# Kernel optimization log

Measured on AMD Instinct MI355X. Metric: run time of the kernel, lower is better.

## Reference

```python
import jax, jax.numpy as jnp
import numpy as np

VOCAB, D_MODEL, N_EXPERTS, TOP_K = 32000, 768, 8, 2
D_FF = 4 * D_MODEL
BATCH, SEQ = 2, 2048


def setup_inputs() -> dict:
    key = jax.random.key(0)
    ks = jax.random.split(key, 6)
    s = 0.02
    return {
        "x": jax.random.randint(ks[0], (BATCH, SEQ), 0, VOCAB),
        "emb": jax.random.normal(ks[1], (VOCAB, D_MODEL), jnp.float32) * s,
        "gate_w": jax.random.normal(ks[2], (D_MODEL, N_EXPERTS), jnp.float32) * s,
        "gate_b": jnp.zeros((N_EXPERTS,), jnp.float32),
        "exp_w": jax.random.normal(ks[3], (N_EXPERTS, D_MODEL, D_FF), jnp.float32) * s,
        "exp_b": jnp.zeros((N_EXPERTS, D_FF), jnp.float32),
        "head_w": jax.random.normal(ks[4], (D_FF, VOCAB), jnp.float32) * s,
        "head_b": jnp.zeros((VOCAB,), jnp.float32),
    }


def reference(x, emb, gate_w, gate_b, exp_w, exp_b, head_w, head_b):
    B, S = x.shape
    h = emb[x]                                   # [B,S,D] embedding gather
    t = h.reshape(B * S, -1)                     # [T,D] token view
    logits = t @ gate_w + gate_b                 # [T,E] router
    topv, topi = jax.lax.top_k(logits, TOP_K)    # top-2 routing
    w = jax.nn.softmax(topv, axis=-1)            # renormalized gate weights
    T = t.shape[0]
    gates = jnp.zeros_like(logits).at[jnp.arange(T)[:, None], topi].set(w)  # [T,E]
    # expert FFN: Linear(d_model -> 4*d_model) + ReLU, dense over experts
    exp_out = jax.nn.relu(jnp.einsum('td,edf->tef', t, exp_w) + exp_b)      # [T,E,F]
    moe = jnp.einsum('te,tef->tf', gates, exp_out)                          # combine
    out = moe @ head_w + head_b                  # [T,V]
    return out.reshape(B, S, -1)
```

## Files before the change

kernel.cpp:

```cpp
#include <hip/hip_runtime.h>

typedef unsigned short u16;
typedef __attribute__((ext_vector_type(8))) short short8;
typedef __attribute__((ext_vector_type(4))) float f32x4;

#define T_TOKENS 4096
#define DMODEL   768
#define DFF      3072
#define NEXP     8
#define NVOCAB   32000

#define EMB_BLOCKS   T_TOKENS
#define TEXP_BX      (DFF / 64)
#define TEXP_BY      (DMODEL / 64)
#define TEXP_BLOCKS  (TEXP_BX * TEXP_BY * NEXP)
#define THEAD_BX     (NVOCAB / 64)
#define THEAD_BY     (DFF / 64)
#define THEAD_BLOCKS (THEAD_BX * THEAD_BY)
#define FRONT_BLOCKS (EMB_BLOCKS + TEXP_BLOCKS + THEAD_BLOCKS)

__device__ __forceinline__ u16 f2bf(float f) {
  unsigned u = __float_as_uint(f);
  u += 0x7FFFu + ((u >> 16) & 1u);
  return (u16)(u >> 16);
}
__device__ __forceinline__ float bf2f(u16 b) {
  return __uint_as_float(((unsigned)b) << 16);
}

__device__ __forceinline__ void async_load16(const void* g, void* lds) {
  __builtin_amdgcn_global_load_lds((const __attribute__((address_space(1))) void*)g,
                                   (__attribute__((address_space(3))) void*)lds, 16, 0, 0);
}

#define SBAR() __builtin_amdgcn_s_barrier()
#define VMCNT(n) asm volatile("s_waitcnt vmcnt(" #n ")")
#define SCHEDB() __builtin_amdgcn_sched_barrier(0)

__device__ __forceinline__ short8 frag(const u16* buf, int row, int kc) {
  return *(const short8*)(buf + (row * 8 + (kc ^ (row & 7))) * 8);
}

__global__ __launch_bounds__(256) void k_front(
    const int* __restrict__ x, const float* __restrict__ emb,
    const float* __restrict__ gw, const float* __restrict__ gb,
    u16* __restrict__ tbf, int* __restrict__ counts,
    int* __restrict__ tlist, float* __restrict__ wlist,
    const float* __restrict__ expw, u16* __restrict__ expwT,
    const float* __restrict__ headw, u16* __restrict__ headwT)
{
  __shared__ float tile[64][65];
  __shared__ float partial[4][NEXP];
  int b = (int)blockIdx.x;

  if (b < EMB_BLOCKS) {
    const int t = b;
    const int tok = x[t];
    const float* er = emb + (size_t)tok * DMODEL;
    float p[NEXP];
#pragma unroll
    for (int e = 0; e < NEXP; ++e) p[e] = 0.f;
#pragma unroll
    for (int i = 0; i < 3; ++i) {
      const int d = threadIdx.x + i * 256;
      const float v = er[d];
      tbf[(size_t)t * DMODEL + d] = f2bf(v);
#pragma unroll
      for (int e = 0; e < NEXP; ++e) p[e] += v * gw[d * NEXP + e];
    }
#pragma unroll
    for (int e = 0; e < NEXP; ++e)
#pragma unroll
      for (int m = 32; m >= 1; m >>= 1) p[e] += __shfl_xor(p[e], m);
    const int lane = threadIdx.x & 63, wv = threadIdx.x >> 6;
    if (lane == 0)
      for (int e = 0; e < NEXP; ++e) partial[wv][e] = p[e];
    __syncthreads();
    if (threadIdx.x == 0) {
      float l[NEXP];
      for (int e = 0; e < NEXP; ++e)
        l[e] = partial[0][e] + partial[1][e] + partial[2][e] + partial[3][e] + gb[e];
      int i0 = 0;
      for (int e = 1; e < NEXP; ++e) if (l[e] > l[i0]) i0 = e;
      int i1 = -1;
      for (int e = 0; e < NEXP; ++e) { if (e == i0) continue; if (i1 < 0 || l[e] > l[i1]) i1 = e; }
      const float w0 = 1.f / (1.f + expf(l[i1] - l[i0]));
      int p0 = atomicAdd(&counts[0 * NEXP + i0], 1);
      tlist[(0 * NEXP + i0) * T_TOKENS + p0] = t;
      wlist[(0 * NEXP + i0) * T_TOKENS + p0] = w0;
      int p1 = atomicAdd(&counts[1 * NEXP + i1], 1);
      tlist[(1 * NEXP + i1) * T_TOKENS + p1] = t;
      wlist[(1 * NEXP + i1) * T_TOKENS + p1] = 1.f - w0;
    }
    return;
  }
  b -= EMB_BLOCKS;

  const float* src; u16* dst; int R, C, bx, by;
  if (b < TEXP_BLOCKS) {
    const int z = b / (TEXP_BX * TEXP_BY);
    const int rem = b - z * (TEXP_BX * TEXP_BY);
    by = rem / TEXP_BX;
    bx = rem - by * TEXP_BX;
    R = DMODEL; C = DFF;
    src = expw + (size_t)z * R * C;
    dst = expwT + (size_t)z * R * C;
  } else {
    b -= TEXP_BLOCKS;
    by = b / THEAD_BX;
    bx = b - by * THEAD_BX;
    R = DFF; C = NVOCAB;
    src = headw;
    dst = headwT;
  }
  {
    const int tx = threadIdx.x & 63, ty = threadIdx.x >> 6;
    const int c = bx * 64 + tx;
#pragma unroll
    for (int i = 0; i < 16; ++i) {
      const int r = by * 64 + ty + i * 4;
      tile[ty + i * 4][tx] = src[(size_t)r * C + c];
    }
    __syncthreads();
    const int h = threadIdx.x & 7;
    const int cl = threadIdx.x >> 3;
    const int rr = by * 64 + h * 8;
#pragma unroll
    for (int i = 0; i < 2; ++i) {
      const int ccl = cl + i * 32;
      const int cc = bx * 64 + ccl;
      short8 pack;
#pragma unroll
      for (int j = 0; j < 8; ++j)
        pack[j] = (short)f2bf(tile[h * 8 + j][ccl]);
      *(short8*)&dst[(size_t)cc * R + rr] = pack;
    }
  }
}

template <int SLOT1>
__global__ __launch_bounds__(256) void k_ffn_slot(
    const u16* __restrict__ tbf, const u16* __restrict__ BT,
    const float* __restrict__ eb, const int* __restrict__ counts,
    const int* __restrict__ tlist, const float* __restrict__ wlist,
    u16* __restrict__ moe)
{
  const int e = blockIdx.z;
  const int cnt = counts[SLOT1 * NEXP + e];
  const int mb = blockIdx.y;
  if (mb * 128 >= cnt) return;
  const int base = (SLOT1 * NEXP + e) * T_TOKENS + mb * 128;
  const int lim = cnt - mb * 128;

  __shared__ u16 aT[2][128 * 64];
  __shared__ u16 bT[2][128 * 64];
  const int tid = threadIdx.x;
  const int wave = tid >> 6, lane = tid & 63;
  const int wm = wave >> 1, wn = wave & 1;
  const int kg = lane >> 4, fr = lane & 15;
  const int n0 = blockIdx.x * 128;
  const u16* Be = BT + (size_t)e * DFF * DMODEL;
  const int K = DMODEL, NT = K / 64;

  int gs8[2], lOf[2]; size_t gBo[2]; int tokA[2][2];
#pragma unroll
  for (int i = 0; i < 2; ++i) {
    const int cch = i * 256 + tid, rl = cch >> 3, sft = cch & 7;
    const int rb = (rl & 31) + ((rl >> 5) << 6);
    gs8[i] = (sft ^ (rl & 7)) * 8;
    lOf[i] = rb * 64 + sft * 8;
    gBo[i] = (size_t)(n0 + rb) * K + gs8[i];
#pragma unroll
    for (int hh = 0; hh < 2; ++hh) {
      const int row = rb + hh * 32;
      tokA[i][hh] = tlist[base + (row < lim ? row : lim - 1)];
    }
  }
  auto stageA = [&](int kb, u16* buf, int h) {
#pragma unroll
    for (int i = 0; i < 2; ++i)
      async_load16(tbf + (size_t)tokA[i][h] * K + kb + gs8[i], buf + lOf[i] + h * 2048);
  };
  auto stageB = [&](int kb, u16* buf, int h) {
#pragma unroll
    for (int i = 0; i < 2; ++i)
      async_load16(Be + gBo[i] + (size_t)(h * 32) * K + kb, buf + lOf[i] + h * 2048);
  };

  f32x4 acc[4][4] = {};
  short8 afA[2][2], afB[2][2], bf[4][2];

  stageA(0, aT[0], 0); stageA(0, aT[0], 1);
  stageB(0, bT[0], 0); stageB(0, bT[0], 1);
  stageA(64, aT[1], 0); stageB(64, bT[1], 0); stageB(64, bT[1], 1);
  VMCNT(6); SCHEDB(); SBAR();
#pragma unroll
  for (int i = 0; i < 2; ++i)
#pragma unroll
    for (int kk = 0; kk < 2; ++kk)
      afA[i][kk] = frag(aT[0], wm * 64 + i * 16 + fr, kk * 4 + kg);
#pragma unroll
  for (int j = 0; j < 4; ++j)
#pragma unroll
    for (int kk = 0; kk < 2; ++kk)
      bf[j][kk] = frag(bT[0], wn * 64 + j * 16 + fr, kk * 4 + kg);

  for (int t = 0; t < NT; ++t) {
    const int cur = t & 1;
    const u16* a_ = aT[cur];
    u16* aw = aT[cur]; u16* bw = bT[cur];
    u16* an = aT[cur ^ 1]; const u16* bn = bT[cur ^ 1];
    const int kb1 = (t + 1) * 64, kb2 = (t + 2) * 64;

    if (t + 1 < NT) stageA(kb1, an, 1);
    __builtin_amdgcn_s_setprio(1);
#pragma unroll
    for (int i = 0; i < 2; ++i)
#pragma unroll
      for (int j = 0; j < 4; ++j)
#pragma unroll
        for (int kk = 0; kk < 2; ++kk)
          acc[i][j] = __builtin_amdgcn_mfma_f32_16x16x32_bf16(afA[i][kk], bf[j][kk], acc[i][j], 0, 0, 0);
    __builtin_amdgcn_s_setprio(0);
#pragma unroll
    for (int i = 0; i < 2; ++i)
#pragma unroll
      for (int kk = 0; kk < 2; ++kk)
        afB[i][kk] = frag(a_, wm * 64 + 32 + i * 16 + fr, kk * 4 + kg);
    if (t + 1 < NT) { VMCNT(2); SCHEDB(); }
    SBAR();

    if (t + 2 < NT) { stageA(kb2, aw, 0); stageB(kb2, bw, 0); stageB(kb2, bw, 1); }
    __builtin_amdgcn_s_setprio(1);
#pragma unroll
    for (int i = 0; i < 2; ++i)
#pragma unroll
      for (int j = 0; j < 4; ++j)
#pragma unroll
        for (int kk = 0; kk < 2; ++kk)
          acc[i + 2][j] = __builtin_amdgcn_mfma_f32_16x16x32_bf16(afB[i][kk], bf[j][kk], acc[i + 2][j], 0, 0, 0);
    __builtin_amdgcn_s_setprio(0);
    if (t + 1 < NT) {
#pragma unroll
      for (int i = 0; i < 2; ++i)
#pragma unroll
        for (int kk = 0; kk < 2; ++kk)
          afA[i][kk] = frag(an, wm * 64 + i * 16 + fr, kk * 4 + kg);
#pragma unroll
      for (int j = 0; j < 4; ++j)
#pragma unroll
        for (int kk = 0; kk < 2; ++kk)
          bf[j][kk] = frag(bn, wn * 64 + j * 16 + fr, kk * 4 + kg);
      if (t + 2 < NT) { VMCNT(6); } else { VMCNT(0); }
      SCHEDB();
    }
    SBAR();
  }

  int trow[4][4]; float wrow[4][4];
#pragma unroll
  for (int i = 0; i < 4; ++i)
#pragma unroll
    for (int r = 0; r < 4; ++r) {
      const int row = wm * 64 + i * 16 + kg * 4 + r;
      if (row < lim) { trow[i][r] = tlist[base + row]; wrow[i][r] = wlist[base + row]; }
      else trow[i][r] = -1;
    }
#pragma unroll
  for (int j = 0; j < 4; ++j) {
    const int col = n0 + wn * 64 + j * 16 + fr;
    const float b = eb[e * DFF + col];
#pragma unroll
    for (int i = 0; i < 4; ++i)
#pragma unroll
      for (int r = 0; r < 4; ++r) {
        if (trow[i][r] < 0) continue;
        float v = acc[i][j][r] + b;
        v = v > 0.f ? v : 0.f;
        v *= wrow[i][r];
        u16* dst = &moe[(size_t)trow[i][r] * DFF + col];
        if (SLOT1) v += bf2f(*dst);
        *dst = f2bf(v);
      }
  }
}

__global__ __launch_bounds__(512, 2) void k_head(
    const u16* __restrict__ A, const u16* __restrict__ BT,
    const float* __restrict__ bias, float* __restrict__ C)
{
  __shared__ u16 aL[2][256 * 64];
  __shared__ u16 bL[2][256 * 64];
  const int tid = threadIdx.x;
  const int lane = tid & 63, wave = tid >> 6;
  const int wm = wave >> 2, wn = wave & 3;
  const int kg = lane >> 4, fr = lane & 15;
  const int wg = (int)blockIdx.x;
  const int swz = (wg & 7) * 250 + (wg >> 3);
  const int m0 = (swz & 15) * 256;
  const int n0 = (swz >> 4) * 256;
  const int K = DFF, NT = K / 64;

  size_t gAo[2], gBo[2]; int lAo[2], lBo[2];
#pragma unroll
  for (int i = 0; i < 2; ++i) {
    const int c = i * 512 + tid, rl = c >> 3, s = c & 7;
    const int rA = (rl & 63) + ((rl >> 6) << 7);
    const int gsA = s ^ (rA & 7);
    gAo[i] = (size_t)(m0 + rA) * K + gsA * 8;
    lAo[i] = rA * 64 + s * 8;
    const int rB = (rl & 31) + ((rl >> 5) << 6);
    const int gsB = s ^ (rB & 7);
    gBo[i] = (size_t)(n0 + rB) * K + gsB * 8;
    lBo[i] = rB * 64 + s * 8;
  }
  auto stageA = [&](int kb, u16* buf, int h) {
#pragma unroll
    for (int i = 0; i < 2; ++i)
      async_load16(A + gAo[i] + (size_t)(h * 64) * K + kb, buf + lAo[i] + h * 4096);
  };
  auto stageB = [&](int kb, u16* buf, int h) {
#pragma unroll
    for (int i = 0; i < 2; ++i)
      async_load16(BT + gBo[i] + (size_t)(h * 32) * K + kb, buf + lBo[i] + h * 2048);
  };

  f32x4 acc[8][4] = {};
  short8 af[4][2], bfl[2][2], bfh[2][2];

  stageA(0, aL[0], 0); stageA(0, aL[0], 1);
  stageB(0, bL[0], 0); stageB(0, bL[0], 1);
  stageA(64, aL[1], 0); stageB(64, bL[1], 0); stageB(64, bL[1], 1);
  VMCNT(6);
  SCHEDB();
  SBAR();
#pragma unroll
  for (int mi = 0; mi < 4; ++mi)
#pragma unroll
    for (int kk = 0; kk < 2; ++kk)
      af[mi][kk] = frag(aL[0], wm * 128 + mi * 16 + fr, kk * 4 + kg);
#pragma unroll
  for (int ni = 0; ni < 2; ++ni)
#pragma unroll
    for (int kk = 0; kk < 2; ++kk) {
      bfl[ni][kk] = frag(bL[0], wn * 64 + ni * 16 + fr, kk * 4 + kg);
      bfh[ni][kk] = frag(bL[0], wn * 64 + 32 + ni * 16 + fr, kk * 4 + kg);
    }

  for (int t = 0; t < NT; ++t) {
    const int cur = t & 1;
    const u16* a_ = aL[cur];
    u16* aw = aL[cur];
    u16* bw = bL[cur];
    u16* an = aL[cur ^ 1];
    const u16* bn = bL[cur ^ 1];
    const int kb1 = (t + 1) * 64, kb2 = (t + 2) * 64;

    if (t + 1 < NT) stageA(kb1, an, 1);
    __builtin_amdgcn_s_setprio(1);
#pragma unroll
    for (int mi = 0; mi < 4; ++mi)
#pragma unroll
      for (int ni = 0; ni < 2; ++ni)
#pragma unroll
        for (int kk = 0; kk < 2; ++kk) {
          acc[mi][ni]     = __builtin_amdgcn_mfma_f32_16x16x32_bf16(af[mi][kk], bfl[ni][kk], acc[mi][ni], 0, 0, 0);
          acc[mi][ni + 2] = __builtin_amdgcn_mfma_f32_16x16x32_bf16(af[mi][kk], bfh[ni][kk], acc[mi][ni + 2], 0, 0, 0);
        }
    __builtin_amdgcn_s_setprio(0);
#pragma unroll
    for (int mi = 0; mi < 4; ++mi)
#pragma unroll
      for (int kk = 0; kk < 2; ++kk)
        af[mi][kk] = frag(a_, wm * 128 + 64 + mi * 16 + fr, kk * 4 + kg);
    if (t + 1 < NT) { VMCNT(2); SCHEDB(); }
    SBAR();

    if (t + 2 < NT) { stageA(kb2, aw, 0); stageB(kb2, bw, 0); stageB(kb2, bw, 1); }
    __builtin_amdgcn_s_setprio(1);
#pragma unroll
    for (int mi = 0; mi < 4; ++mi)
#pragma unroll
      for (int ni = 0; ni < 2; ++ni)
#pragma unroll
        for (int kk = 0; kk < 2; ++kk) {
          acc[mi + 4][ni]     = __builtin_amdgcn_mfma_f32_16x16x32_bf16(af[mi][kk], bfl[ni][kk], acc[mi + 4][ni], 0, 0, 0);
          acc[mi + 4][ni + 2] = __builtin_amdgcn_mfma_f32_16x16x32_bf16(af[mi][kk], bfh[ni][kk], acc[mi + 4][ni + 2], 0, 0, 0);
        }
    __builtin_amdgcn_s_setprio(0);
    if (t + 1 < NT) {
#pragma unroll
      for (int mi = 0; mi < 4; ++mi)
#pragma unroll
        for (int kk = 0; kk < 2; ++kk)
          af[mi][kk] = frag(an, wm * 128 + mi * 16 + fr, kk * 4 + kg);
#pragma unroll
      for (int ni = 0; ni < 2; ++ni)
#pragma unroll
        for (int kk = 0; kk < 2; ++kk) {
          bfl[ni][kk] = frag(bn, wn * 64 + ni * 16 + fr, kk * 4 + kg);
          bfh[ni][kk] = frag(bn, wn * 64 + 32 + ni * 16 + fr, kk * 4 + kg);
        }
      if (t + 2 < NT) { VMCNT(6); } else { VMCNT(0); }
      SCHEDB();
    }
    SBAR();
  }

#pragma unroll
  for (int ni = 0; ni < 4; ++ni) {
    const int col = n0 + wn * 64 + ni * 16 + fr;
    const float b = bias[col];
#pragma unroll
    for (int mi = 0; mi < 8; ++mi) {
      const int row = m0 + wm * 128 + (mi >> 2) * 64 + (mi & 3) * 16 + kg * 4;
#pragma unroll
      for (int r = 0; r < 4; ++r)
        __builtin_nontemporal_store(acc[mi][ni][r] + b,
                                    &C[(size_t)(row + r) * NVOCAB + col]);
    }
  }
}

extern "C" void kernel_launch(void* const* d_in, const int* in_sizes, int n_in,
                              void* d_out, int out_size, void* d_ws, size_t ws_size,
                              hipStream_t stream) {
  const int*   x     = (const int*)d_in[0];
  const float* emb   = (const float*)d_in[1];
  const float* gw    = (const float*)d_in[2];
  const float* gb    = (const float*)d_in[3];
  const float* expw  = (const float*)d_in[4];
  const float* expb  = (const float*)d_in[5];
  const float* headw = (const float*)d_in[6];
  const float* headb = (const float*)d_in[7];
  float* out = (float*)d_out;

  char* ws = (char*)d_ws;
  size_t off = 0;
  auto alloc = [&](size_t bytes) { size_t r = off; off += (bytes + 255) & ~(size_t)255; return r; };
  u16*   tbf    = (u16*)(ws + alloc((size_t)T_TOKENS * DMODEL * 2));
  int*   counts = (int*)(ws + alloc(2 * NEXP * 4));
  int*   tlist  = (int*)(ws + alloc((size_t)2 * NEXP * T_TOKENS * 4));
  float* wlist  = (float*)(ws + alloc((size_t)2 * NEXP * T_TOKENS * 4));
  u16*   expwT  = (u16*)(ws + alloc((size_t)NEXP * DFF * DMODEL * 2));
  u16*   headwT = (u16*)(ws + alloc((size_t)NVOCAB * DFF * 2));
  u16*   moe    = (u16*)(ws + alloc((size_t)T_TOKENS * DFF * 2));

  hipMemsetAsync(counts, 0, 2 * NEXP * 4, stream);
  k_front<<<FRONT_BLOCKS, 256, 0, stream>>>(x, emb, gw, gb, tbf, counts, tlist, wlist,
                                            expw, expwT, headw, headwT);
  k_ffn_slot<0><<<dim3(DFF / 128, T_TOKENS / 128, NEXP), 256, 0, stream>>>(
      tbf, expwT, expb, counts, tlist, wlist, moe);
  k_ffn_slot<1><<<dim3(DFF / 128, T_TOKENS / 128, NEXP), 256, 0, stream>>>(
      tbf, expwT, expb, counts, tlist, wlist, moe);
  k_head<<<(T_TOKENS / 256) * (NVOCAB / 256), 512, 0, stream>>>(moe, headwT, headb, out);
}
```

Baseline: 1.166 ms.

## Merge both routing-slot FFN launches into one grid with separate output buffers

```diff
diff --git a/kernel.cpp b/kernel.cpp
--- a/kernel.cpp
+++ b/kernel.cpp
@@ -138,19 +138,20 @@
   }
 }
 
-template <int SLOT1>
-__global__ __launch_bounds__(256) void k_ffn_slot(
+__global__ __launch_bounds__(256) void k_ffn(
     const u16* __restrict__ tbf, const u16* __restrict__ BT,
     const float* __restrict__ eb, const int* __restrict__ counts,
     const int* __restrict__ tlist, const float* __restrict__ wlist,
-    u16* __restrict__ moe)
+    u16* __restrict__ moe0, u16* __restrict__ moe1)
 {
-  const int e = blockIdx.z;
-  const int cnt = counts[SLOT1 * NEXP + e];
+  const int z = blockIdx.z;
+  const int e = z & 7;
+  const int cnt = counts[z];
   const int mb = blockIdx.y;
   if (mb * 128 >= cnt) return;
-  const int base = (SLOT1 * NEXP + e) * T_TOKENS + mb * 128;
+  const int base = z * T_TOKENS + mb * 128;
   const int lim = cnt - mb * 128;
+  u16* __restrict__ dstbuf = (z >= NEXP) ? moe1 : moe0;
 
   __shared__ u16 aT[2][128 * 64];
   __shared__ u16 bT[2][128 * 64];
@@ -278,10 +279,24 @@
         float v = acc[i][j][r] + b;
         v = v > 0.f ? v : 0.f;
         v *= wrow[i][r];
-        u16* dst = &moe[(size_t)trow[i][r] * DFF + col];
-        if (SLOT1) v += bf2f(*dst);
-        *dst = f2bf(v);
+        dstbuf[(size_t)trow[i][r] * DFF + col] = f2bf(v);
       }
+  }
+}
+
+__global__ __launch_bounds__(256) void k_combine(
+    u16* __restrict__ m0, const u16* __restrict__ m1)
+{
+  const size_t n = (size_t)T_TOKENS * DFF / 8;
+  for (size_t i = (size_t)blockIdx.x * 256 + threadIdx.x; i < n;
+       i += (size_t)gridDim.x * 256) {
+    short8 a = ((const short8*)m0)[i];
+    short8 b = ((const short8*)m1)[i];
+    short8 o;
+#pragma unroll
+    for (int j = 0; j < 8; ++j)
+      o[j] = (short)f2bf(bf2f((u16)a[j]) + bf2f((u16)b[j]));
+    ((short8*)m0)[i] = o;
   }
 }
 
@@ -444,14 +459,14 @@
   float* wlist  = (float*)(ws + alloc((size_t)2 * NEXP * T_TOKENS * 4));
   u16*   expwT  = (u16*)(ws + alloc((size_t)NEXP * DFF * DMODEL * 2));
   u16*   headwT = (u16*)(ws + alloc((size_t)NVOCAB * DFF * 2));
-  u16*   moe    = (u16*)(ws + alloc((size_t)T_TOKENS * DFF * 2));
+  u16*   moe0   = (u16*)(ws + alloc((size_t)T_TOKENS * DFF * 2));
+  u16*   moe1   = (u16*)(ws + alloc((size_t)T_TOKENS * DFF * 2));
 
   hipMemsetAsync(counts, 0, 2 * NEXP * 4, stream);
   k_front<<<FRONT_BLOCKS, 256, 0, stream>>>(x, emb, gw, gb, tbf, counts, tlist, wlist,
                                             expw, expwT, headw, headwT);
-  k_ffn_slot<0><<<dim3(DFF / 128, T_TOKENS / 128, NEXP), 256, 0, stream>>>(
-      tbf, expwT, expb, counts, tlist, wlist, moe);
-  k_ffn_slot<1><<<dim3(DFF / 128, T_TOKENS / 128, NEXP), 256, 0, stream>>>(
-      tbf, expwT, expb, counts, tlist, wlist, moe);
-  k_head<<<(T_TOKENS / 256) * (NVOCAB / 256), 512, 0, stream>>>(moe, headwT, headb, out);
-}
+  k_ffn<<<dim3(DFF / 128, T_TOKENS / 128, 2 * NEXP), 256, 0, stream>>>(
+      tbf, expwT, expb, counts, tlist, wlist, moe0, moe1);
+  k_combine<<<2048, 256, 0, stream>>>(moe0, moe1);
+  k_head<<<(T_TOKENS / 256) * (NVOCAB / 256), 512, 0, stream>>>(moe0, headwT, headb, out);
+}
```

Measured after the change: 1.169 ms. Within noise of the previous version (+0.3%).
